# Performance work log

Measured on AMD Instinct MI355X. Metric: run time of the kernel, lower is better.

The kernel has to match this reference:

```python
import jax, jax.numpy as jnp
import numpy as np

N_NODES = 10000
N_EDGES = 640000
NF = 128
HID = 128
NORM_FACTOR = 100.0


def setup_inputs() -> dict:
    key = jax.random.key(0)
    ks = jax.random.split(key, 8)
    s = lambda fan_in: 1.0 / np.sqrt(fan_in)
    return {
        "h": jax.random.normal(ks[0], (N_NODES, NF), dtype=jnp.float32),
        "edge_index": jax.random.randint(ks[1], (2, N_EDGES), 0, N_NODES, dtype=jnp.int64),
        "ew1": jax.random.normal(ks[2], (2 * NF, HID), dtype=jnp.float32) * s(2 * NF),
        "eb1": jnp.zeros((HID,), dtype=jnp.float32),
        "ew2": jax.random.normal(ks[3], (HID, HID), dtype=jnp.float32) * s(HID),
        "eb2": jnp.zeros((HID,), dtype=jnp.float32),
        "nw1": jax.random.normal(ks[4], (HID + NF, HID), dtype=jnp.float32) * s(HID + NF),
        "nb1": jnp.zeros((HID,), dtype=jnp.float32),
        "nw2": jax.random.normal(ks[5], (HID, NF), dtype=jnp.float32) * s(HID),
        "nb2": jnp.zeros((NF,), dtype=jnp.float32),
    }


def reference(h, edge_index, ew1, eb1, ew2, eb2, nw1, nb1, nw2, nb2):
    row, col = edge_index[0], edge_index[1]
    # edge model: gather endpoints, concat, 2-layer SiLU MLP -> mij [E, HID]
    x = jnp.concatenate([h[row], h[col]], axis=1)          # [E, 2*NF]
    mij = jax.nn.silu(x @ ew1 + eb1)
    mij = jax.nn.silu(mij @ ew2 + eb2)                     # [E, HID]
    # aggregation: scatter-add messages to source nodes, 'sum' normalization
    agg = jax.ops.segment_sum(mij, row, num_segments=h.shape[0]) / NORM_FACTOR
    # node model: residual MLP update
    a = jnp.concatenate([h, agg], axis=1)                  # [V, NF+HID]
    out = h + (jax.nn.silu(a @ nw1 + nb1) @ nw2 + nb2)     # [V, NF]
    return out, mij
```

## Files before the change

### kernel.cpp

```cpp
#include <hip/hip_runtime.h>

typedef __attribute__((ext_vector_type(8))) short short8;
typedef __attribute__((ext_vector_type(4))) float f32x4;
typedef unsigned short ushort_t;
typedef unsigned int uint_t;

#define MFMA16(a, b, c) __builtin_amdgcn_mfma_f32_16x16x32_bf16((a), (b), (c), 0, 0, 0)

constexpr int V = 10000;
constexpr int E = 640000;
constexpr int NF = 128;
constexpr int XS_STRIDE = 264;
constexpr int YS_STRIDE = 136;

__device__ __forceinline__ ushort_t f2b(float f) {
    uint_t u = __float_as_uint(f);
    u += 0x7FFFu + ((u >> 16) & 1u);
    return (ushort_t)(u >> 16);
}

__device__ __forceinline__ float silu(float x) {
    return x / (1.0f + __expf(-x));
}

__global__ void cvt_f32_bf16(const float* __restrict__ src, ushort_t* __restrict__ dst, int n) {
    int i = blockIdx.x * blockDim.x + threadIdx.x;
    if (i < n) dst[i] = f2b(src[i]);
}

__global__ __launch_bounds__(256, 2) void edge_kernel(
    const ushort_t* __restrict__ hb, const int* __restrict__ eidx,
    const ushort_t* __restrict__ w1, const float* __restrict__ eb1,
    const ushort_t* __restrict__ w2, const float* __restrict__ eb2,
    float* __restrict__ mij, float* __restrict__ agg) {
    __shared__ __align__(16) ushort_t xs[64 * XS_STRIDE];
    __shared__ __align__(16) ushort_t ys[64 * YS_STRIDE];
    __shared__ int ridx[64];

    const int tid = threadIdx.x;
    const int wave = tid >> 6;
    const int lane = tid & 63;
    const int quad = lane >> 4;
    const int ln = lane & 15;
    const int ncol0 = wave * 32;

    short8 b1f[8][2];
    short8 b2f[4][2];
#pragma unroll
    for (int kk = 0; kk < 8; kk++)
#pragma unroll
        for (int t = 0; t < 2; t++) {
            short8 f;
#pragma unroll
            for (int j = 0; j < 8; j++)
                f[j] = ((const short*)w1)[(kk * 32 + quad * 8 + j) * 128 + ncol0 + t * 16 + ln];
            b1f[kk][t] = f;
        }
#pragma unroll
    for (int kk = 0; kk < 4; kk++)
#pragma unroll
        for (int t = 0; t < 2; t++) {
            short8 f;
#pragma unroll
            for (int j = 0; j < 8; j++)
                f[j] = ((const short*)w2)[(kk * 32 + quad * 8 + j) * 128 + ncol0 + t * 16 + ln];
            b2f[kk][t] = f;
        }
    const float bv1[2] = {eb1[ncol0 + ln], eb1[ncol0 + 16 + ln]};
    const float bv2[2] = {eb2[ncol0 + ln], eb2[ncol0 + 16 + ln]};

    for (int tile = blockIdx.x; tile < E / 64; tile += gridDim.x) {
        const int e0 = tile * 64;
        {
            const int e = tid >> 2, seg = tid & 3;
            const int r = eidx[e0 + e];
            const int c = eidx[E + e0 + e];
            if (seg == 0) ridx[e] = r;
            const int node = (seg < 2) ? r : c;
            const uint4* src = (const uint4*)(hb + node * 128 + (seg & 1) * 64);
            uint4* dst = (uint4*)(xs + e * XS_STRIDE + seg * 64);
#pragma unroll
            for (int u = 0; u < 8; u++) dst[u] = src[u];
        }
        __syncthreads();

        f32x4 acc[4][2];
#pragma unroll
        for (int mt = 0; mt < 4; mt++)
#pragma unroll
            for (int t = 0; t < 2; t++) acc[mt][t] = f32x4{bv1[t], bv1[t], bv1[t], bv1[t]};
#pragma unroll
        for (int kk = 0; kk < 8; kk++) {
#pragma unroll
            for (int mt = 0; mt < 4; mt++) {
                short8 a = *(const short8*)(xs + (mt * 16 + ln) * XS_STRIDE + kk * 32 + quad * 8);
                acc[mt][0] = MFMA16(a, b1f[kk][0], acc[mt][0]);
                acc[mt][1] = MFMA16(a, b1f[kk][1], acc[mt][1]);
            }
        }
#pragma unroll
        for (int mt = 0; mt < 4; mt++)
#pragma unroll
            for (int t = 0; t < 2; t++) {
#pragma unroll
                for (int r = 0; r < 4; r++) {
                    float s = silu(acc[mt][t][r]);
                    ys[(mt * 16 + quad * 4 + r) * YS_STRIDE + ncol0 + t * 16 + ln] = f2b(s);
                }
            }
        __syncthreads();

        f32x4 acc2[4][2];
#pragma unroll
        for (int mt = 0; mt < 4; mt++)
#pragma unroll
            for (int t = 0; t < 2; t++) acc2[mt][t] = f32x4{bv2[t], bv2[t], bv2[t], bv2[t]};
#pragma unroll
        for (int kk = 0; kk < 4; kk++) {
#pragma unroll
            for (int mt = 0; mt < 4; mt++) {
                short8 a = *(const short8*)(ys + (mt * 16 + ln) * YS_STRIDE + kk * 32 + quad * 8);
                acc2[mt][0] = MFMA16(a, b2f[kk][0], acc2[mt][0]);
                acc2[mt][1] = MFMA16(a, b2f[kk][1], acc2[mt][1]);
            }
        }

#pragma unroll
        for (int mt = 0; mt < 4; mt++) {
#pragma unroll
            for (int r = 0; r < 4; r++) {
                const int row = mt * 16 + quad * 4 + r;
                const int nsrc = ridx[row];
#pragma unroll
                for (int t = 0; t < 2; t++) {
                    float s = silu(acc2[mt][t][r]);
                    const int col = ncol0 + t * 16 + ln;
                    mij[(size_t)(e0 + row) * 128 + col] = s;
                    unsafeAtomicAdd(&agg[nsrc * 128 + col], s);
                }
            }
        }
        __syncthreads();
    }
}

__global__ __launch_bounds__(256, 2) void node_kernel(
    const ushort_t* __restrict__ hb, const float* __restrict__ h32,
    const float* __restrict__ agg,
    const ushort_t* __restrict__ w1, const float* __restrict__ nb1,
    const ushort_t* __restrict__ w2, const float* __restrict__ nb2,
    float* __restrict__ out) {
    __shared__ __align__(16) ushort_t xs[64 * XS_STRIDE];
    __shared__ __align__(16) ushort_t ys[64 * YS_STRIDE];

    const int tid = threadIdx.x;
    const int wave = tid >> 6;
    const int lane = tid & 63;
    const int quad = lane >> 4;
    const int ln = lane & 15;
    const int ncol0 = wave * 32;
    const int i0 = blockIdx.x * 64;

    short8 b1f[8][2];
    short8 b2f[4][2];
#pragma unroll
    for (int kk = 0; kk < 8; kk++)
#pragma unroll
        for (int t = 0; t < 2; t++) {
            short8 f;
#pragma unroll
            for (int j = 0; j < 8; j++)
                f[j] = ((const short*)w1)[(kk * 32 + quad * 8 + j) * 128 + ncol0 + t * 16 + ln];
            b1f[kk][t] = f;
        }
#pragma unroll
    for (int kk = 0; kk < 4; kk++)
#pragma unroll
        for (int t = 0; t < 2; t++) {
            short8 f;
#pragma unroll
            for (int j = 0; j < 8; j++)
                f[j] = ((const short*)w2)[(kk * 32 + quad * 8 + j) * 128 + ncol0 + t * 16 + ln];
            b2f[kk][t] = f;
        }
    const float bv1[2] = {nb1[ncol0 + ln], nb1[ncol0 + 16 + ln]};
    const float bv2[2] = {nb2[ncol0 + ln], nb2[ncol0 + 16 + ln]};

    {
        const int e = tid >> 2, seg = tid & 3;
        const int node = i0 + e;
        if (node < V) {
            if (seg < 2) {
                const uint4* src = (const uint4*)(hb + node * 128 + seg * 64);
                uint4* dst = (uint4*)(xs + e * XS_STRIDE + seg * 64);
#pragma unroll
                for (int u = 0; u < 8; u++) dst[u] = src[u];
            } else {
                const float4* src = (const float4*)(agg + node * 128 + (seg & 1) * 64);
                ushort4* dst = (ushort4*)(xs + e * XS_STRIDE + seg * 64);
#pragma unroll
                for (int u = 0; u < 16; u++) {
                    float4 v = src[u];
                    ushort4 o;
                    o.x = f2b(v.x * 0.01f);
                    o.y = f2b(v.y * 0.01f);
                    o.z = f2b(v.z * 0.01f);
                    o.w = f2b(v.w * 0.01f);
                    dst[u] = o;
                }
            }
        } else {
            uint4 z{0, 0, 0, 0};
            uint4* dst = (uint4*)(xs + e * XS_STRIDE + seg * 64);
#pragma unroll
            for (int u = 0; u < 8; u++) dst[u] = z;
        }
    }
    __syncthreads();

    f32x4 acc[4][2];
#pragma unroll
    for (int mt = 0; mt < 4; mt++)
#pragma unroll
        for (int t = 0; t < 2; t++) acc[mt][t] = f32x4{bv1[t], bv1[t], bv1[t], bv1[t]};
#pragma unroll
    for (int kk = 0; kk < 8; kk++) {
#pragma unroll
        for (int mt = 0; mt < 4; mt++) {
            short8 a = *(const short8*)(xs + (mt * 16 + ln) * XS_STRIDE + kk * 32 + quad * 8);
            acc[mt][0] = MFMA16(a, b1f[kk][0], acc[mt][0]);
            acc[mt][1] = MFMA16(a, b1f[kk][1], acc[mt][1]);
        }
    }
#pragma unroll
    for (int mt = 0; mt < 4; mt++)
#pragma unroll
        for (int t = 0; t < 2; t++) {
#pragma unroll
            for (int r = 0; r < 4; r++) {
                float s = silu(acc[mt][t][r]);
                ys[(mt * 16 + quad * 4 + r) * YS_STRIDE + ncol0 + t * 16 + ln] = f2b(s);
            }
        }
    __syncthreads();

    f32x4 acc2[4][2];
#pragma unroll
    for (int mt = 0; mt < 4; mt++)
#pragma unroll
        for (int t = 0; t < 2; t++) acc2[mt][t] = f32x4{bv2[t], bv2[t], bv2[t], bv2[t]};
#pragma unroll
    for (int kk = 0; kk < 4; kk++) {
#pragma unroll
        for (int mt = 0; mt < 4; mt++) {
            short8 a = *(const short8*)(ys + (mt * 16 + ln) * YS_STRIDE + kk * 32 + quad * 8);
            acc2[mt][0] = MFMA16(a, b2f[kk][0], acc2[mt][0]);
            acc2[mt][1] = MFMA16(a, b2f[kk][1], acc2[mt][1]);
        }
    }
#pragma unroll
    for (int mt = 0; mt < 4; mt++) {
#pragma unroll
        for (int r = 0; r < 4; r++) {
            const int row = mt * 16 + quad * 4 + r;
            const int node = i0 + row;
            if (node < V) {
#pragma unroll
                for (int t = 0; t < 2; t++) {
                    const int col = ncol0 + t * 16 + ln;
                    out[(size_t)node * 128 + col] = h32[(size_t)node * 128 + col] + acc2[mt][t][r];
                }
            }
        }
    }
}

extern "C" void kernel_launch(void* const* d_in, const int* in_sizes, int n_in,
                              void* d_out, int out_size, void* d_ws, size_t ws_size,
                              hipStream_t stream) {
    const float* h = (const float*)d_in[0];
    const int* eidx = (const int*)d_in[1];
    const float* ew1 = (const float*)d_in[2];
    const float* eb1 = (const float*)d_in[3];
    const float* ew2 = (const float*)d_in[4];
    const float* eb2 = (const float*)d_in[5];
    const float* nw1 = (const float*)d_in[6];
    const float* nb1 = (const float*)d_in[7];
    const float* nw2 = (const float*)d_in[8];
    const float* nb2 = (const float*)d_in[9];

    float* out = (float*)d_out;
    float* mij = (float*)d_out + (size_t)V * 128;

    uint8_t* ws = (uint8_t*)d_ws;
    ushort_t* hb = (ushort_t*)(ws);
    ushort_t* w1b = (ushort_t*)(ws + 2560000);
    ushort_t* w2b = (ushort_t*)(ws + 2560000 + 65536);
    ushort_t* nw1b = (ushort_t*)(ws + 2560000 + 98304);
    ushort_t* nw2b = (ushort_t*)(ws + 2560000 + 163840);
    float* agg = (float*)(ws + 2560000 + 196608);

    hipMemsetAsync(agg, 0, (size_t)V * 128 * sizeof(float), stream);

    cvt_f32_bf16<<<(V * 128 + 255) / 256, 256, 0, stream>>>(h, hb, V * 128);
    cvt_f32_bf16<<<128, 256, 0, stream>>>(ew1, w1b, 256 * 128);
    cvt_f32_bf16<<<64, 256, 0, stream>>>(ew2, w2b, 128 * 128);
    cvt_f32_bf16<<<128, 256, 0, stream>>>(nw1, nw1b, 256 * 128);
    cvt_f32_bf16<<<64, 256, 0, stream>>>(nw2, nw2b, 128 * 128);

    edge_kernel<<<2048, 256, 0, stream>>>(hb, eidx, w1b, eb1, w2b, eb2, mij, agg);
    node_kernel<<<(V + 63) / 64, 256, 0, stream>>>(hb, h, agg, nw1b, nb1, nw2b, nb2, out);
}
```

Measured before the change: 598.5 us.

## Fuse prep launches, alias edge LDS buffers, raise occupancy, shrink node tiles

Replaces the memset and five conversion launches with one vectorized prep kernel that also zeroes the aggregation buffer. The edge kernel reuses its input LDS tile for the hidden activations, with an extra barrier, and asks for four blocks per CU instead of two. The node kernel processes 16 nodes per block, so more blocks are launched, and drops the bounds checks because 16 divides V. The higher launch bound may squeeze registers, since each thread holds all weight fragments, which risks spills in the edge kernel.

```diff
diff --git a/kernel.cpp b/kernel.cpp
--- a/kernel.cpp
+++ b/kernel.cpp
@@ -9,7 +9,6 @@
 
 constexpr int V = 10000;
 constexpr int E = 640000;
-constexpr int NF = 128;
 constexpr int XS_STRIDE = 264;
 constexpr int YS_STRIDE = 136;
 
@@ -23,19 +22,47 @@
     return x / (1.0f + __expf(-x));
 }
 
-__global__ void cvt_f32_bf16(const float* __restrict__ src, ushort_t* __restrict__ dst, int n) {
+constexpr int H4 = V * 128 / 4;
+constexpr int W14 = 256 * 128 / 4;
+constexpr int W24 = 128 * 128 / 4;
+constexpr int AGG4 = V * 128 / 4;
+constexpr int PREP_TOTAL = H4 + 2 * W14 + 2 * W24 + AGG4;
+
+__device__ __forceinline__ void cvt4(const float* __restrict__ s, ushort_t* __restrict__ d, int i) {
+    float4 v = ((const float4*)s)[i];
+    ushort4 o;
+    o.x = f2b(v.x); o.y = f2b(v.y); o.z = f2b(v.z); o.w = f2b(v.w);
+    ((ushort4*)d)[i] = o;
+}
+
+__global__ void prep_kernel(const float* __restrict__ h,
+                            const float* __restrict__ ew1, const float* __restrict__ ew2,
+                            const float* __restrict__ nw1, const float* __restrict__ nw2,
+                            ushort_t* __restrict__ hb, ushort_t* __restrict__ w1b,
+                            ushort_t* __restrict__ w2b, ushort_t* __restrict__ nw1b,
+                            ushort_t* __restrict__ nw2b, float* __restrict__ agg) {
     int i = blockIdx.x * blockDim.x + threadIdx.x;
-    if (i < n) dst[i] = f2b(src[i]);
-}
-
-__global__ __launch_bounds__(256, 2) void edge_kernel(
+    if (i < H4) { cvt4(h, hb, i); return; }
+    i -= H4;
+    if (i < W14) { cvt4(ew1, w1b, i); return; }
+    i -= W14;
+    if (i < W24) { cvt4(ew2, w2b, i); return; }
+    i -= W24;
+    if (i < W14) { cvt4(nw1, nw1b, i); return; }
+    i -= W14;
+    if (i < W24) { cvt4(nw2, nw2b, i); return; }
+    i -= W24;
+    if (i < AGG4) ((float4*)agg)[i] = float4{0.f, 0.f, 0.f, 0.f};
+}
+
+__global__ __launch_bounds__(256, 4) void edge_kernel(
     const ushort_t* __restrict__ hb, const int* __restrict__ eidx,
     const ushort_t* __restrict__ w1, const float* __restrict__ eb1,
     const ushort_t* __restrict__ w2, const float* __restrict__ eb2,
     float* __restrict__ mij, float* __restrict__ agg) {
     __shared__ __align__(16) ushort_t xs[64 * XS_STRIDE];
-    __shared__ __align__(16) ushort_t ys[64 * YS_STRIDE];
     __shared__ int ridx[64];
+    ushort_t* ys = xs;
 
     const int tid = threadIdx.x;
     const int wave = tid >> 6;
@@ -98,6 +125,8 @@
                 acc[mt][1] = MFMA16(a, b1f[kk][1], acc[mt][1]);
             }
         }
+        __syncthreads();
+
 #pragma unroll
         for (int mt = 0; mt < 4; mt++)
 #pragma unroll
@@ -144,14 +173,14 @@
     }
 }
 
-__global__ __launch_bounds__(256, 2) void node_kernel(
+__global__ __launch_bounds__(256, 4) void node_kernel(
     const ushort_t* __restrict__ hb, const float* __restrict__ h32,
     const float* __restrict__ agg,
     const ushort_t* __restrict__ w1, const float* __restrict__ nb1,
     const ushort_t* __restrict__ w2, const float* __restrict__ nb2,
     float* __restrict__ out) {
-    __shared__ __align__(16) ushort_t xs[64 * XS_STRIDE];
-    __shared__ __align__(16) ushort_t ys[64 * YS_STRIDE];
+    __shared__ __align__(16) ushort_t xs[16 * XS_STRIDE];
+    ushort_t* ys = xs;
 
     const int tid = threadIdx.x;
     const int wave = tid >> 6;
@@ -159,7 +188,7 @@
     const int quad = lane >> 4;
     const int ln = lane & 15;
     const int ncol0 = wave * 32;
-    const int i0 = blockIdx.x * 64;
+    const int i0 = blockIdx.x * 16;
 
     short8 b1f[8][2];
     short8 b2f[4][2];
@@ -187,90 +216,63 @@
     const float bv2[2] = {nb2[ncol0 + ln], nb2[ncol0 + 16 + ln]};
 
     {
-        const int e = tid >> 2, seg = tid & 3;
-        const int node = i0 + e;
-        if (node < V) {
-            if (seg < 2) {
-                const uint4* src = (const uint4*)(hb + node * 128 + seg * 64);
-                uint4* dst = (uint4*)(xs + e * XS_STRIDE + seg * 64);
-#pragma unroll
-                for (int u = 0; u < 8; u++) dst[u] = src[u];
-            } else {
-                const float4* src = (const float4*)(agg + node * 128 + (seg & 1) * 64);
-                ushort4* dst = (ushort4*)(xs + e * XS_STRIDE + seg * 64);
-#pragma unroll
-                for (int u = 0; u < 16; u++) {
-                    float4 v = src[u];
-                    ushort4 o;
-                    o.x = f2b(v.x * 0.01f);
-                    o.y = f2b(v.y * 0.01f);
-                    o.z = f2b(v.z * 0.01f);
-                    o.w = f2b(v.w * 0.01f);
-                    dst[u] = o;
-                }
-            }
+        const int r = tid >> 4, chunk = tid & 15;
+        const int node = i0 + r;
+        if (chunk < 8) {
+            const uint4* src = (const uint4*)(hb + node * 128 + chunk * 16);
+            uint4* dst = (uint4*)(xs + r * XS_STRIDE + chunk * 16);
+            dst[0] = src[0];
+            dst[1] = src[1];
         } else {
-            uint4 z{0, 0, 0, 0};
-            uint4* dst = (uint4*)(xs + e * XS_STRIDE + seg * 64);
-#pragma unroll
-            for (int u = 0; u < 8; u++) dst[u] = z;
+            const float4* src = (const float4*)(agg + node * 128 + (chunk - 8) * 16);
+            ushort4* dst = (ushort4*)(xs + r * XS_STRIDE + 128 + (chunk - 8) * 16);
+#pragma unroll
+            for (int u = 0; u < 4; u++) {
+                float4 v = src[u];
+                ushort4 o;
+                o.x = f2b(v.x * 0.01f);
+                o.y = f2b(v.y * 0.01f);
+                o.z = f2b(v.z * 0.01f);
+                o.w = f2b(v.w * 0.01f);
+                dst[u] = o;
+            }
         }
     }
     __syncthreads();
 
-    f32x4 acc[4][2];
-#pragma unroll
-    for (int mt = 0; mt < 4; mt++)
-#pragma unroll
-        for (int t = 0; t < 2; t++) acc[mt][t] = f32x4{bv1[t], bv1[t], bv1[t], bv1[t]};
+    f32x4 acc[2];
+    acc[0] = f32x4{bv1[0], bv1[0], bv1[0], bv1[0]};
+    acc[1] = f32x4{bv1[1], bv1[1], bv1[1], bv1[1]};
 #pragma unroll
     for (int kk = 0; kk < 8; kk++) {
-#pragma unroll
-        for (int mt = 0; mt < 4; mt++) {
-            short8 a = *(const short8*)(xs + (mt * 16 + ln) * XS_STRIDE + kk * 32 + quad * 8);
-            acc[mt][0] = MFMA16(a, b1f[kk][0], acc[mt][0]);
-            acc[mt][1] = MFMA16(a, b1f[kk][1], acc[mt][1]);
-        }
-    }
-#pragma unroll
-    for (int mt = 0; mt < 4; mt++)
-#pragma unroll
-        for (int t = 0; t < 2; t++) {
-#pragma unroll
-            for (int r = 0; r < 4; r++) {
-                float s = silu(acc[mt][t][r]);
-                ys[(mt * 16 + quad * 4 + r) * YS_STRIDE + ncol0 + t * 16 + ln] = f2b(s);
-            }
-        }
+        short8 a = *(const short8*)(xs + ln * XS_STRIDE + kk * 32 + quad * 8);
+        acc[0] = MFMA16(a, b1f[kk][0], acc[0]);
+        acc[1] = MFMA16(a, b1f[kk][1], acc[1]);
+    }
     __syncthreads();
-
-    f32x4 acc2[4][2];
-#pragma unroll
-    for (int mt = 0; mt < 4; mt++)
-#pragma unroll
-        for (int t = 0; t < 2; t++) acc2[mt][t] = f32x4{bv2[t], bv2[t], bv2[t], bv2[t]};
+#pragma unroll
+    for (int t = 0; t < 2; t++)
+#pragma unroll
+        for (int r = 0; r < 4; r++)
+            ys[(quad * 4 + r) * YS_STRIDE + ncol0 + t * 16 + ln] = f2b(silu(acc[t][r]));
+    __syncthreads();
+
+    f32x4 acc2[2];
+    acc2[0] = f32x4{bv2[0], bv2[0], bv2[0], bv2[0]};
+    acc2[1] = f32x4{bv2[1], bv2[1], bv2[1], bv2[1]};
 #pragma unroll
     for (int kk = 0; kk < 4; kk++) {
-#pragma unroll
-        for (int mt = 0; mt < 4; mt++) {
-            short8 a = *(const short8*)(ys + (mt * 16 + ln) * YS_STRIDE + kk * 32 + quad * 8);
-            acc2[mt][0] = MFMA16(a, b2f[kk][0], acc2[mt][0]);
-            acc2[mt][1] = MFMA16(a, b2f[kk][1], acc2[mt][1]);
-        }
-    }
-#pragma unroll
-    for (int mt = 0; mt < 4; mt++) {
-#pragma unroll
-        for (int r = 0; r < 4; r++) {
-            const int row = mt * 16 + quad * 4 + r;
-            const int node = i0 + row;
-            if (node < V) {
-#pragma unroll
-                for (int t = 0; t < 2; t++) {
-                    const int col = ncol0 + t * 16 + ln;
-                    out[(size_t)node * 128 + col] = h32[(size_t)node * 128 + col] + acc2[mt][t][r];
-                }
-            }
+        short8 a = *(const short8*)(ys + ln * YS_STRIDE + kk * 32 + quad * 8);
+        acc2[0] = MFMA16(a, b2f[kk][0], acc2[0]);
+        acc2[1] = MFMA16(a, b2f[kk][1], acc2[1]);
+    }
+#pragma unroll
+    for (int r = 0; r < 4; r++) {
+        const int node = i0 + quad * 4 + r;
+#pragma unroll
+        for (int t = 0; t < 2; t++) {
+            const int col = ncol0 + t * 16 + ln;
+            out[(size_t)node * 128 + col] = h32[(size_t)node * 128 + col] + acc2[t][r];
         }
     }
 }
@@ -300,14 +302,8 @@
     ushort_t* nw2b = (ushort_t*)(ws + 2560000 + 163840);
     float* agg = (float*)(ws + 2560000 + 196608);
 
-    hipMemsetAsync(agg, 0, (size_t)V * 128 * sizeof(float), stream);
-
-    cvt_f32_bf16<<<(V * 128 + 255) / 256, 256, 0, stream>>>(h, hb, V * 128);
-    cvt_f32_bf16<<<128, 256, 0, stream>>>(ew1, w1b, 256 * 128);
-    cvt_f32_bf16<<<64, 256, 0, stream>>>(ew2, w2b, 128 * 128);
-    cvt_f32_bf16<<<128, 256, 0, stream>>>(nw1, nw1b, 256 * 128);
-    cvt_f32_bf16<<<64, 256, 0, stream>>>(nw2, nw2b, 128 * 128);
-
+    prep_kernel<<<(PREP_TOTAL + 255) / 256, 256, 0, stream>>>(
+        h, ew1, ew2, nw1, nw2, hb, w1b, w2b, nw1b, nw2b, agg);
     edge_kernel<<<2048, 256, 0, stream>>>(hb, eidx, w1b, eb1, w2b, eb2, mij, agg);
-    node_kernel<<<(V + 63) / 64, 256, 0, stream>>>(hb, h, agg, nw1b, nb1, nw2b, nb2, out);
-}
+    node_kernel<<<V / 16, 256, 0, stream>>>(hb, h, agg, nw1b, nb1, nw2b, nb2, out);
+}
```

Measured after the change: 671.8 us. 12.3% more time.
